# Performance work log

Hardware: AMD Instinct MI355X
Metric: run time of the kernel (lower is better)

The kernel has to match this reference:

```python
import jax, jax.numpy as jnp
import numpy as np

N, IN_DIM, H, K = 4096, 64, 64, 3
DT = 0.05


def graph_filter(z, S_powers, W):
    # z: [N, d_in], S_powers: [K, N, N], W: [K, d_in, d_out]
    zk = jnp.einsum('knm,md->knd', S_powers, z)   # K-hop diffused features
    return jnp.einsum('knd,kde->ne', zk, W)       # sum over taps k


def setup_inputs() -> dict:
    key = jax.random.key(0)
    ks = jax.random.split(key, 8)
    w_scale = 0.1
    return {
        'x': jax.random.normal(ks[0], (N, H), jnp.float32),
        'u': jax.random.normal(ks[1], (N, IN_DIM), jnp.float32),
        'S_powers': jax.random.normal(ks[2], (K, N, N), jnp.float32) / np.float32(np.sqrt(N)),
        'WA_hat': jax.random.normal(ks[3], (K, H, H), jnp.float32) * w_scale,
        'WB_hat': jax.random.normal(ks[4], (K, IN_DIM, H), jnp.float32) * w_scale,
        'WA_state': jax.random.normal(ks[5], (K, H, H), jnp.float32) * w_scale,
        'WB_state': jax.random.normal(ks[6], (K, IN_DIM, H), jnp.float32) * w_scale,
        'bx': jnp.zeros((1, H), jnp.float32),
        'bu': jnp.zeros((1, H), jnp.float32),
        'b': jnp.ones((1, H), jnp.float32) * 0.1,
        'n_steps': 4,
    }


def reference(x, u, S_powers, WA_hat, WB_hat, WA_state, WB_state, bx, bu, b, n_steps):
    # Input-driven terms are constant across solver steps; hoist them.
    fu = jax.nn.relu(graph_filter(u, S_powers, WB_hat) + bu)   # [N, H]
    sigma_c = jnp.tanh(graph_filter(u, S_powers, WB_state))    # [N, H]

    def step(xc, _):
        f = jax.nn.relu(graph_filter(xc, S_powers, WA_hat) + bx) + fu
        dx = -(b + f) * xc - graph_filter(xc, S_powers, WA_state) + f * sigma_c
        xn = jnp.clip(xc + DT * dx, -1.0, 1.0)
        return xn, None

    xf, _ = jax.lax.scan(step, x, None, length=n_steps)
    return xf
```

## Files before the change

kernel.cpp:

```cpp
#include <hip/hip_runtime.h>
#include <math.h>


typedef unsigned short u16;
typedef unsigned int u32;
typedef __attribute__((ext_vector_type(8))) short short8;
typedef __attribute__((ext_vector_type(4))) float f32x4;

#define NN 4096
#define HD 64
#define KB32 128
#define DT_C 0.05f

__device__ __forceinline__ u16 f2bf(float f) {
    u32 u = __float_as_uint(f);
    u += 0x7FFFu + ((u >> 16) & 1u);
    return (u16)(u >> 16);
}
__device__ __forceinline__ u32 pk2(float a, float b) {
    return (u32)f2bf(a) | ((u32)f2bf(b) << 16);
}

__global__ __launch_bounds__(256) void convS_kernel(
    const float* __restrict__ S, u16* __restrict__ SbT)
{
    const int slab = blockIdx.y;
    const int tap = slab >> 7, kb = slab & 127;
    const int t = threadIdx.x;
    const int n = blockIdx.x * 64 + (t >> 2);
    const int kq = (t & 3) * 8;
    const float* src = S + ((size_t)tap * NN + n) * NN + kb * 32 + kq;
    float4 f0 = ((const float4*)src)[0];
    float4 f1 = ((const float4*)src)[1];
    uint4 o;
    o.x = pk2(f0.x, f0.y); o.y = pk2(f0.z, f0.w);
    o.z = pk2(f1.x, f1.y); o.w = pk2(f1.z, f1.w);
    *(uint4*)(SbT + ((size_t)slab * NN + n) * 32 + kq) = o;
}

__global__ __launch_bounds__(256) void zprep_kernel(
    const float* __restrict__ u, const float* __restrict__ x,
    const float* __restrict__ WAh, const float* __restrict__ WAs,
    const float* __restrict__ WBh, const float* __restrict__ WBs,
    u16* __restrict__ utT, u16* __restrict__ xtT, u16* __restrict__ WtT)
{
    const int b = blockIdx.x;
    const int t = threadIdx.x;
    if (b < 256) {
        const float* z = (b < 128) ? u : x;
        u16* ztT = (b < 128) ? utT : xtT;
        const int kb = b & 127, n0 = kb * 32;
        __shared__ __align__(16) u16 tile[64][40];
        const int nl = t >> 3, c0 = (t & 7) * 8;
        const float* src = z + (size_t)(n0 + nl) * HD + c0;
        float4 f0 = ((const float4*)src)[0];
        float4 f1 = ((const float4*)src)[1];
        tile[c0 + 0][nl] = f2bf(f0.x); tile[c0 + 1][nl] = f2bf(f0.y);
        tile[c0 + 2][nl] = f2bf(f0.z); tile[c0 + 3][nl] = f2bf(f0.w);
        tile[c0 + 4][nl] = f2bf(f1.x); tile[c0 + 5][nl] = f2bf(f1.y);
        tile[c0 + 6][nl] = f2bf(f1.z); tile[c0 + 7][nl] = f2bf(f1.w);
        __syncthreads();
        const int e = t >> 2, kw0 = (t & 3) * 8;
        short8 v = *(const short8*)&tile[e][kw0];
        *(short8*)(ztT + ((size_t)kb * 64 + e) * 32 + kw0) = v;
    } else {
        for (int f = t; f < 4 * 6 * 64 * 32; f += 256) {
            int mat = f / 12288, r = f % 12288;
            int s = r / 2048, r2 = r % 2048;
            int e = r2 >> 5, kw = r2 & 31;
            int kp = s * 32 + kw, tap = kp >> 6, d = kp & 63;
            const float* Wm = (mat == 0) ? WAh : (mat == 1) ? WAs : (mat == 2) ? WBh : WBs;
            WtT[f] = f2bf(Wm[((size_t)tap * HD + d) * HD + e]);
        }
    }
}

__global__ __launch_bounds__(256) void pack_kernel(
    const float* __restrict__ xn, u16* __restrict__ xtT)
{
    const int kb = blockIdx.x, n0 = kb * 32;
    const int t = threadIdx.x;
    __shared__ __align__(16) u16 tile[64][40];
    const int nl = t >> 3, c0 = (t & 7) * 8;
    const float* src = xn + (size_t)(n0 + nl) * HD + c0;
    float4 f0 = ((const float4*)src)[0];
    float4 f1 = ((const float4*)src)[1];
    tile[c0 + 0][nl] = f2bf(f0.x); tile[c0 + 1][nl] = f2bf(f0.y);
    tile[c0 + 2][nl] = f2bf(f0.z); tile[c0 + 3][nl] = f2bf(f0.w);
    tile[c0 + 4][nl] = f2bf(f1.x); tile[c0 + 5][nl] = f2bf(f1.y);
    tile[c0 + 6][nl] = f2bf(f1.z); tile[c0 + 7][nl] = f2bf(f1.w);
    __syncthreads();
    const int e = t >> 2, kw0 = (t & 3) * 8;
    short8 v = *(const short8*)&tile[e][kw0];
    *(short8*)(xtT + ((size_t)kb * 64 + e) * 32 + kw0) = v;
}

__global__ __launch_bounds__(256) void diffuseA_kernel(
    const u16* __restrict__ SbT, const u16* __restrict__ utT,
    const u16* __restrict__ xtT, float* __restrict__ Yp, int iters)
{
    const int t = threadIdx.x;
    const int tap = blockIdx.z;
    const int row0 = blockIdx.x * 128;
    const int kb0 = blockIdx.y * iters;
    const int w = t >> 6, lane = t & 63, l15 = lane & 15, quad = lane >> 4;

    const u16* A0 = SbT + (((size_t)(tap * KB32) * NN + row0 + w * 32 + l15) * 32) + quad * 8;
    const size_t arowstride = (size_t)NN * 32;
    const u16* Bu = utT + (size_t)(l15)*0;

    f32x4 z4 = {0.f, 0.f, 0.f, 0.f};
    f32x4 acc[2][2][4];
    #pragma unroll
    for (int s = 0; s < 2; ++s)
        #pragma unroll
        for (int i = 0; i < 2; ++i)
            #pragma unroll
            for (int j = 0; j < 4; ++j) acc[s][i][j] = z4;

    #pragma unroll 2
    for (int it = 0; it < iters; ++it) {
        const int kb = kb0 + it;
        const u16* ab = A0 + (size_t)kb * arowstride;
        short8 a0 = *(const short8*)(ab);
        short8 a1 = *(const short8*)(ab + 16 * 32);
        #pragma unroll
        for (int ct = 0; ct < 4; ++ct) {
            const size_t bo = ((size_t)kb * 64 + ct * 16 + l15) * 32 + quad * 8;
            short8 bu = *(const short8*)(utT + bo);
            short8 bx = *(const short8*)(xtT + bo);
            acc[0][0][ct] = __builtin_amdgcn_mfma_f32_16x16x32_bf16(a0, bu, acc[0][0][ct], 0, 0, 0);
            acc[0][1][ct] = __builtin_amdgcn_mfma_f32_16x16x32_bf16(a1, bu, acc[0][1][ct], 0, 0, 0);
            acc[1][0][ct] = __builtin_amdgcn_mfma_f32_16x16x32_bf16(a0, bx, acc[1][0][ct], 0, 0, 0);
            acc[1][1][ct] = __builtin_amdgcn_mfma_f32_16x16x32_bf16(a1, bx, acc[1][1][ct], 0, 0, 0);
        }
    }
    (void)Bu;
    #pragma unroll
    for (int s = 0; s < 2; ++s) {
        float* yb = Yp + ((size_t)((blockIdx.y * 3 + tap) * 2 + s) * NN + row0) * HD;
        #pragma unroll
        for (int rt = 0; rt < 2; ++rt)
            #pragma unroll
            for (int ct = 0; ct < 4; ++ct)
                #pragma unroll
                for (int r = 0; r < 4; ++r)
                    yb[(size_t)(w * 32 + rt * 16 + quad * 4 + r) * HD + ct * 16 + l15] = acc[s][rt][ct][r];
    }
}

__global__ __launch_bounds__(256) void diffuseS_kernel(
    const u16* __restrict__ SbT, const u16* __restrict__ xtT,
    float* __restrict__ Yp, int iters)
{
    const int t = threadIdx.x;
    const int tap = blockIdx.z;
    const int row0 = blockIdx.x * 128;
    const int kb0 = blockIdx.y * iters;
    const int w = t >> 6, lane = t & 63, l15 = lane & 15, quad = lane >> 4;

    const u16* A0 = SbT + (((size_t)(tap * KB32) * NN + row0 + w * 32 + l15) * 32) + quad * 8;
    const size_t arowstride = (size_t)NN * 32;

    f32x4 z4 = {0.f, 0.f, 0.f, 0.f};
    f32x4 acc[2][4];
    #pragma unroll
    for (int i = 0; i < 2; ++i)
        #pragma unroll
        for (int j = 0; j < 4; ++j) acc[i][j] = z4;

    #pragma unroll 2
    for (int it = 0; it < iters; ++it) {
        const int kb = kb0 + it;
        const u16* ab = A0 + (size_t)kb * arowstride;
        short8 a0 = *(const short8*)(ab);
        short8 a1 = *(const short8*)(ab + 16 * 32);
        #pragma unroll
        for (int ct = 0; ct < 4; ++ct) {
            short8 bb = *(const short8*)(xtT + ((size_t)kb * 64 + ct * 16 + l15) * 32 + quad * 8);
            acc[0][ct] = __builtin_amdgcn_mfma_f32_16x16x32_bf16(a0, bb, acc[0][ct], 0, 0, 0);
            acc[1][ct] = __builtin_amdgcn_mfma_f32_16x16x32_bf16(a1, bb, acc[1][ct], 0, 0, 0);
        }
    }
    float* yb = Yp + ((size_t)(blockIdx.y * 3 + tap) * NN + row0) * HD;
    #pragma unroll
    for (int rt = 0; rt < 2; ++rt)
        #pragma unroll
        for (int ct = 0; ct < 4; ++ct)
            #pragma unroll
            for (int r = 0; r < 4; ++r)
                yb[(size_t)(w * 32 + rt * 16 + quad * 4 + r) * HD + ct * 16 + l15] = acc[rt][ct][r];
}

__global__ __launch_bounds__(256) void reduce_kernel(
    const float* __restrict__ Yp, int KS, int nsrc,
    u16* __restrict__ dst0, u16* __restrict__ dst1)
{
    const int tg = blockIdx.x * 256 + threadIdx.x;
    const int src = tg / 98304;
    const int r = tg - src * 98304;
    const int tap = r >> 15;
    const int r2 = r & 32767;
    const int n = r2 >> 3;
    const int dg = (r2 & 7) * 8;
    const float* p = Yp + (((size_t)tap * nsrc + src) * NN + n) * HD + dg;
    const size_t kstride = (size_t)3 * nsrc * NN * HD;
    float4 s0 = {0.f, 0.f, 0.f, 0.f}, s1 = {0.f, 0.f, 0.f, 0.f};
    for (int ks = 0; ks < KS; ++ks) {
        float4 v0 = ((const float4*)(p + ks * kstride))[0];
        float4 v1 = ((const float4*)(p + ks * kstride))[1];
        s0.x += v0.x; s0.y += v0.y; s0.z += v0.z; s0.w += v0.w;
        s1.x += v1.x; s1.y += v1.y; s1.z += v1.z; s1.w += v1.w;
    }
    u16* dst = src ? dst1 : dst0;
    uint4 o;
    o.x = pk2(s0.x, s0.y); o.y = pk2(s0.z, s0.w);
    o.z = pk2(s1.x, s1.y); o.w = pk2(s1.z, s1.w);
    *(uint4*)(dst + (((size_t)(tap * 2 + (dg >> 5)) * NN + n) * 32) + (dg & 31)) = o;
}

__global__ __launch_bounds__(64) void update_step_kernel(
    const u16* __restrict__ YxT, const u16* __restrict__ WtT,
    const float* __restrict__ bx, const float* __restrict__ bvec,
    const float* __restrict__ fu, const float* __restrict__ sc,
    const float* __restrict__ xc, float* __restrict__ xn)
{
    const int n0 = blockIdx.x * 16;
    const int lane = threadIdx.x, l15 = lane & 15, quad = lane >> 4;

    f32x4 z4 = {0.f, 0.f, 0.f, 0.f};
    f32x4 aF[4], aG[4];
    #pragma unroll
    for (int ct = 0; ct < 4; ++ct) { aF[ct] = z4; aG[ct] = z4; }
    #pragma unroll
    for (int s = 0; s < 6; ++s) {
        short8 a = *(const short8*)(YxT + (((size_t)s * NN + n0 + l15) * 32) + quad * 8);
        #pragma unroll
        for (int ct = 0; ct < 4; ++ct) {
            const size_t wo = (((size_t)(0 * 6 + s) * 64) + ct * 16 + l15) * 32 + quad * 8;
            short8 bF = *(const short8*)(WtT + wo);
            short8 bG = *(const short8*)(WtT + wo + 6 * 64 * 32);
            aF[ct] = __builtin_amdgcn_mfma_f32_16x16x32_bf16(a, bF, aF[ct], 0, 0, 0);
            aG[ct] = __builtin_amdgcn_mfma_f32_16x16x32_bf16(a, bG, aG[ct], 0, 0, 0);
        }
    }
    #pragma unroll
    for (int ct = 0; ct < 4; ++ct) {
        const int e = ct * 16 + l15;
        const float bxv = bx[e], bbv = bvec[e];
        #pragma unroll
        for (int r = 0; r < 4; ++r) {
            const int n = n0 + quad * 4 + r;
            const size_t o = (size_t)n * HD + e;
            float f = fmaxf(aF[ct][r] + bxv, 0.f) + fu[o];
            float g = aG[ct][r];
            float xv = xc[o];
            float dx = -(bbv + f) * xv - g + f * sc[o];
            xn[o] = fminf(fmaxf(xv + DT_C * dx, -1.f), 1.f);
        }
    }
}

__global__ __launch_bounds__(64) void update1_kernel(
    const u16* __restrict__ YuT, const u16* __restrict__ YxT,
    const u16* __restrict__ WtT,
    const float* __restrict__ bx, const float* __restrict__ bu,
    const float* __restrict__ bvec, const float* __restrict__ x0,
    float* __restrict__ fu, float* __restrict__ sc, float* __restrict__ x1)
{
    const int n0 = blockIdx.x * 16;
    const int lane = threadIdx.x, l15 = lane & 15, quad = lane >> 4;

    f32x4 z4 = {0.f, 0.f, 0.f, 0.f};
    f32x4 aFu[4], aSc[4], aF[4], aG[4];
    #pragma unroll
    for (int ct = 0; ct < 4; ++ct) { aFu[ct] = z4; aSc[ct] = z4; aF[ct] = z4; aG[ct] = z4; }
    #pragma unroll
    for (int s = 0; s < 6; ++s) {
        const size_t ao = (((size_t)s * NN + n0 + l15) * 32) + quad * 8;
        short8 au = *(const short8*)(YuT + ao);
        short8 ax = *(const short8*)(YxT + ao);
        #pragma unroll
        for (int ct = 0; ct < 4; ++ct) {
            const size_t wo = (((size_t)s * 64) + ct * 16 + l15) * 32 + quad * 8;
            short8 bF  = *(const short8*)(WtT + wo);
            short8 bG  = *(const short8*)(WtT + wo + 6 * 64 * 32);
            short8 bFu = *(const short8*)(WtT + wo + 2 * 6 * 64 * 32);
            short8 bSc = *(const short8*)(WtT + wo + 3 * 6 * 64 * 32);
            aF[ct]  = __builtin_amdgcn_mfma_f32_16x16x32_bf16(ax, bF,  aF[ct],  0, 0, 0);
            aG[ct]  = __builtin_amdgcn_mfma_f32_16x16x32_bf16(ax, bG,  aG[ct],  0, 0, 0);
            aFu[ct] = __builtin_amdgcn_mfma_f32_16x16x32_bf16(au, bFu, aFu[ct], 0, 0, 0);
            aSc[ct] = __builtin_amdgcn_mfma_f32_16x16x32_bf16(au, bSc, aSc[ct], 0, 0, 0);
        }
    }
    #pragma unroll
    for (int ct = 0; ct < 4; ++ct) {
        const int e = ct * 16 + l15;
        const float bxv = bx[e], buv = bu[e], bbv = bvec[e];
        #pragma unroll
        for (int r = 0; r < 4; ++r) {
            const int n = n0 + quad * 4 + r;
            const size_t o = (size_t)n * HD + e;
            float fuv = fmaxf(aFu[ct][r] + buv, 0.f);
            float scv = tanhf(aSc[ct][r]);
            float f = fmaxf(aF[ct][r] + bxv, 0.f) + fuv;
            float g = aG[ct][r];
            float xv = x0[o];
            float dx = -(bbv + f) * xv - g + f * scv;
            fu[o] = fuv; sc[o] = scv;
            x1[o] = fminf(fmaxf(xv + DT_C * dx, -1.f), 1.f);
        }
    }
}

extern "C" void kernel_launch(void* const* d_in, const int* in_sizes, int n_in,
                              void* d_out, int out_size, void* d_ws, size_t ws_size,
                              hipStream_t stream) {
    const float* x   = (const float*)d_in[0];
    const float* u   = (const float*)d_in[1];
    const float* S   = (const float*)d_in[2];
    const float* WAh = (const float*)d_in[3];
    const float* WBh = (const float*)d_in[4];
    const float* WAs = (const float*)d_in[5];
    const float* WBs = (const float*)d_in[6];
    const float* bx  = (const float*)d_in[7];
    const float* bu  = (const float*)d_in[8];
    const float* bvec= (const float*)d_in[9];
    float* out = (float*)d_out;

    const size_t sbf_bytes = (size_t)3 * NN * NN * 2;
    const size_t slice = (size_t)NN * HD * 4;
    const size_t rest = 2 * 524288 + 98304 + 2 * 1572864 + 4 * 1048576;
    int KS_A = 4, KS_S = 8;
    if (ws_size < sbf_bytes + 24 * slice + rest) { KS_A = 2; KS_S = 4; }
    if (ws_size < sbf_bytes + 12 * slice + rest) { KS_A = 1; KS_S = 2; }
    const int nslice = (KS_A * 6 > KS_S * 3) ? KS_A * 6 : KS_S * 3;

    char* p = (char*)d_ws;
    u16* SbT  = (u16*)p;         p += sbf_bytes;
    float* Yp = (float*)p;       p += (size_t)nslice * slice;
    u16* utT  = (u16*)p;         p += 524288;
    u16* xtT  = (u16*)p;         p += 524288;
    u16* WtT  = (u16*)p;         p += 98304;
    u16* YuT  = (u16*)p;         p += 1572864;
    u16* YxT  = (u16*)p;         p += 1572864;
    float* fu = (float*)p;       p += 1048576;
    float* sc = (float*)p;       p += 1048576;
    float* xA = (float*)p;       p += 1048576;
    float* xB = (float*)p;       p += 1048576;

    zprep_kernel<<<257, 256, 0, stream>>>(u, x, WAh, WAs, WBh, WBs, utT, xtT, WtT);
    convS_kernel<<<dim3(64, 384), 256, 0, stream>>>(S, SbT);

    diffuseA_kernel<<<dim3(32, KS_A, 3), 256, 0, stream>>>(SbT, utT, xtT, Yp, KB32 / KS_A);
    reduce_kernel<<<768, 256, 0, stream>>>(Yp, KS_A, 2, YuT, YxT);
    update1_kernel<<<256, 64, 0, stream>>>(YuT, YxT, WtT, bx, bu, bvec, x, fu, sc, xA);
    pack_kernel<<<128, 256, 0, stream>>>(xA, xtT);
    diffuseS_kernel<<<dim3(32, KS_S, 3), 256, 0, stream>>>(SbT, xtT, Yp, KB32 / KS_S);
    reduce_kernel<<<384, 256, 0, stream>>>(Yp, KS_S, 1, YxT, YxT);
    update_step_kernel<<<256, 64, 0, stream>>>(YxT, WtT, bx, bvec, fu, sc, xA, xB);
    pack_kernel<<<128, 256, 0, stream>>>(xB, xtT);

    diffuseS_kernel<<<dim3(32, KS_S, 3), 256, 0, stream>>>(SbT, xtT, Yp, KB32 / KS_S);
    reduce_kernel<<<384, 256, 0, stream>>>(Yp, KS_S, 1, YxT, YxT);
    update_step_kernel<<<256, 64, 0, stream>>>(YxT, WtT, bx, bvec, fu, sc, xB, xA);
    pack_kernel<<<128, 256, 0, stream>>>(xA, xtT);

    diffuseS_kernel<<<dim3(32, KS_S, 3), 256, 0, stream>>>(SbT, xtT, Yp, KB32 / KS_S);
    reduce_kernel<<<384, 256, 0, stream>>>(Yp, KS_S, 1, YxT, YxT);
    update_step_kernel<<<256, 64, 0, stream>>>(YxT, WtT, bx, bvec, fu, sc, xA, out);
}
```

Before: 534.8 us.

## Fuse S conversion into first diffusion and reduce/pack into update kernels

The separate fp32→bf16 conversion of S is folded into the first diffusion kernel, which reads fp32 S directly, converts it in registers, feeds MFMA and writes the bf16 copy for later steps. The split-K reduce and the bf16 repack of the new state are folded into the update kernels, which now use 256 threads, stage partial sums in LDS and write the packed transposed x themselves. This removes several launches and intermediate round-trips through global memory. In exchange the first diffusion kernel becomes heavier on memory traffic and conversion work, and each update block redoes the split-K sum for its own rows.

Result: faster. 491.6 us (-8.1%).

```diff
diff --git a/kernel.cpp b/kernel.cpp
--- a/kernel.cpp
+++ b/kernel.cpp
@@ -19,23 +19,6 @@
 }
 __device__ __forceinline__ u32 pk2(float a, float b) {
     return (u32)f2bf(a) | ((u32)f2bf(b) << 16);
-}
-
-__global__ __launch_bounds__(256) void convS_kernel(
-    const float* __restrict__ S, u16* __restrict__ SbT)
-{
-    const int slab = blockIdx.y;
-    const int tap = slab >> 7, kb = slab & 127;
-    const int t = threadIdx.x;
-    const int n = blockIdx.x * 64 + (t >> 2);
-    const int kq = (t & 3) * 8;
-    const float* src = S + ((size_t)tap * NN + n) * NN + kb * 32 + kq;
-    float4 f0 = ((const float4*)src)[0];
-    float4 f1 = ((const float4*)src)[1];
-    uint4 o;
-    o.x = pk2(f0.x, f0.y); o.y = pk2(f0.z, f0.w);
-    o.z = pk2(f1.x, f1.y); o.w = pk2(f1.z, f1.w);
-    *(uint4*)(SbT + ((size_t)slab * NN + n) * 32 + kq) = o;
 }
 
 __global__ __launch_bounds__(256) void zprep_kernel(
@@ -75,29 +58,10 @@
     }
 }
 
-__global__ __launch_bounds__(256) void pack_kernel(
-    const float* __restrict__ xn, u16* __restrict__ xtT)
-{
-    const int kb = blockIdx.x, n0 = kb * 32;
-    const int t = threadIdx.x;
-    __shared__ __align__(16) u16 tile[64][40];
-    const int nl = t >> 3, c0 = (t & 7) * 8;
-    const float* src = xn + (size_t)(n0 + nl) * HD + c0;
-    float4 f0 = ((const float4*)src)[0];
-    float4 f1 = ((const float4*)src)[1];
-    tile[c0 + 0][nl] = f2bf(f0.x); tile[c0 + 1][nl] = f2bf(f0.y);
-    tile[c0 + 2][nl] = f2bf(f0.z); tile[c0 + 3][nl] = f2bf(f0.w);
-    tile[c0 + 4][nl] = f2bf(f1.x); tile[c0 + 5][nl] = f2bf(f1.y);
-    tile[c0 + 6][nl] = f2bf(f1.z); tile[c0 + 7][nl] = f2bf(f1.w);
-    __syncthreads();
-    const int e = t >> 2, kw0 = (t & 3) * 8;
-    short8 v = *(const short8*)&tile[e][kw0];
-    *(short8*)(xtT + ((size_t)kb * 64 + e) * 32 + kw0) = v;
-}
-
 __global__ __launch_bounds__(256) void diffuseA_kernel(
-    const u16* __restrict__ SbT, const u16* __restrict__ utT,
-    const u16* __restrict__ xtT, float* __restrict__ Yp, int iters)
+    const float* __restrict__ S, const u16* __restrict__ utT,
+    const u16* __restrict__ xtT, u16* __restrict__ SbT,
+    float* __restrict__ Yp, int iters)
 {
     const int t = threadIdx.x;
     const int tap = blockIdx.z;
@@ -105,9 +69,9 @@
     const int kb0 = blockIdx.y * iters;
     const int w = t >> 6, lane = t & 63, l15 = lane & 15, quad = lane >> 4;
 
-    const u16* A0 = SbT + (((size_t)(tap * KB32) * NN + row0 + w * 32 + l15) * 32) + quad * 8;
-    const size_t arowstride = (size_t)NN * 32;
-    const u16* Bu = utT + (size_t)(l15)*0;
+    const int r0 = row0 + w * 32 + l15;
+    const float* Sb = S + ((size_t)tap * NN + r0) * NN + quad * 8;
+    u16* Wb = SbT + (((size_t)tap * KB32) * NN + r0) * 32 + quad * 8;
 
     f32x4 z4 = {0.f, 0.f, 0.f, 0.f};
     f32x4 acc[2][2][4];
@@ -117,6 +81,68 @@
         for (int i = 0; i < 2; ++i)
             #pragma unroll
             for (int j = 0; j < 4; ++j) acc[s][i][j] = z4;
+
+    #pragma unroll 2
+    for (int it = 0; it < iters; ++it) {
+        const int kb = kb0 + it;
+        const float* sp0 = Sb + (size_t)kb * 32;
+        const float* sp1 = sp0 + (size_t)16 * NN;
+        float4 f0 = ((const float4*)sp0)[0];
+        float4 f1 = ((const float4*)sp0)[1];
+        float4 g0 = ((const float4*)sp1)[0];
+        float4 g1 = ((const float4*)sp1)[1];
+        union U { uint4 u4; short8 s8; };
+        U A0, A1;
+        A0.u4.x = pk2(f0.x, f0.y); A0.u4.y = pk2(f0.z, f0.w);
+        A0.u4.z = pk2(f1.x, f1.y); A0.u4.w = pk2(f1.z, f1.w);
+        A1.u4.x = pk2(g0.x, g0.y); A1.u4.y = pk2(g0.z, g0.w);
+        A1.u4.z = pk2(g1.x, g1.y); A1.u4.w = pk2(g1.z, g1.w);
+        u16* wb = Wb + (size_t)kb * (NN * 32);
+        *(uint4*)wb = A0.u4;
+        *(uint4*)(wb + 16 * 32) = A1.u4;
+        #pragma unroll
+        for (int ct = 0; ct < 4; ++ct) {
+            const size_t bo = ((size_t)kb * 64 + ct * 16 + l15) * 32 + quad * 8;
+            short8 bu = *(const short8*)(utT + bo);
+            short8 bx = *(const short8*)(xtT + bo);
+            acc[0][0][ct] = __builtin_amdgcn_mfma_f32_16x16x32_bf16(A0.s8, bu, acc[0][0][ct], 0, 0, 0);
+            acc[0][1][ct] = __builtin_amdgcn_mfma_f32_16x16x32_bf16(A1.s8, bu, acc[0][1][ct], 0, 0, 0);
+            acc[1][0][ct] = __builtin_amdgcn_mfma_f32_16x16x32_bf16(A0.s8, bx, acc[1][0][ct], 0, 0, 0);
+            acc[1][1][ct] = __builtin_amdgcn_mfma_f32_16x16x32_bf16(A1.s8, bx, acc[1][1][ct], 0, 0, 0);
+        }
+    }
+    #pragma unroll
+    for (int s = 0; s < 2; ++s) {
+        float* yb = Yp + ((size_t)((blockIdx.y * 3 + tap) * 2 + s) * NN + row0) * HD;
+        #pragma unroll
+        for (int rt = 0; rt < 2; ++rt)
+            #pragma unroll
+            for (int ct = 0; ct < 4; ++ct)
+                #pragma unroll
+                for (int r = 0; r < 4; ++r)
+                    yb[(size_t)(w * 32 + rt * 16 + quad * 4 + r) * HD + ct * 16 + l15] = acc[s][rt][ct][r];
+    }
+}
+
+__global__ __launch_bounds__(256) void diffuseS_kernel(
+    const u16* __restrict__ SbT, const u16* __restrict__ xtT,
+    float* __restrict__ Yp, int iters)
+{
+    const int t = threadIdx.x;
+    const int tap = blockIdx.z;
+    const int row0 = blockIdx.x * 128;
+    const int kb0 = blockIdx.y * iters;
+    const int w = t >> 6, lane = t & 63, l15 = lane & 15, quad = lane >> 4;
+
+    const u16* A0 = SbT + (((size_t)(tap * KB32) * NN + row0 + w * 32 + l15) * 32) + quad * 8;
+    const size_t arowstride = (size_t)NN * 32;
+
+    f32x4 z4 = {0.f, 0.f, 0.f, 0.f};
+    f32x4 acc[2][4];
+    #pragma unroll
+    for (int i = 0; i < 2; ++i)
+        #pragma unroll
+        for (int j = 0; j < 4; ++j) acc[i][j] = z4;
 
     #pragma unroll 2
     for (int it = 0; it < iters; ++it) {
@@ -126,57 +152,6 @@
         short8 a1 = *(const short8*)(ab + 16 * 32);
         #pragma unroll
         for (int ct = 0; ct < 4; ++ct) {
-            const size_t bo = ((size_t)kb * 64 + ct * 16 + l15) * 32 + quad * 8;
-            short8 bu = *(const short8*)(utT + bo);
-            short8 bx = *(const short8*)(xtT + bo);
-            acc[0][0][ct] = __builtin_amdgcn_mfma_f32_16x16x32_bf16(a0, bu, acc[0][0][ct], 0, 0, 0);
-            acc[0][1][ct] = __builtin_amdgcn_mfma_f32_16x16x32_bf16(a1, bu, acc[0][1][ct], 0, 0, 0);
-            acc[1][0][ct] = __builtin_amdgcn_mfma_f32_16x16x32_bf16(a0, bx, acc[1][0][ct], 0, 0, 0);
-            acc[1][1][ct] = __builtin_amdgcn_mfma_f32_16x16x32_bf16(a1, bx, acc[1][1][ct], 0, 0, 0);
-        }
-    }
-    (void)Bu;
-    #pragma unroll
-    for (int s = 0; s < 2; ++s) {
-        float* yb = Yp + ((size_t)((blockIdx.y * 3 + tap) * 2 + s) * NN + row0) * HD;
-        #pragma unroll
-        for (int rt = 0; rt < 2; ++rt)
-            #pragma unroll
-            for (int ct = 0; ct < 4; ++ct)
-                #pragma unroll
-                for (int r = 0; r < 4; ++r)
-                    yb[(size_t)(w * 32 + rt * 16 + quad * 4 + r) * HD + ct * 16 + l15] = acc[s][rt][ct][r];
-    }
-}
-
-__global__ __launch_bounds__(256) void diffuseS_kernel(
-    const u16* __restrict__ SbT, const u16* __restrict__ xtT,
-    float* __restrict__ Yp, int iters)
-{
-    const int t = threadIdx.x;
-    const int tap = blockIdx.z;
-    const int row0 = blockIdx.x * 128;
-    const int kb0 = blockIdx.y * iters;
-    const int w = t >> 6, lane = t & 63, l15 = lane & 15, quad = lane >> 4;
-
-    const u16* A0 = SbT + (((size_t)(tap * KB32) * NN + row0 + w * 32 + l15) * 32) + quad * 8;
-    const size_t arowstride = (size_t)NN * 32;
-
-    f32x4 z4 = {0.f, 0.f, 0.f, 0.f};
-    f32x4 acc[2][4];
-    #pragma unroll
-    for (int i = 0; i < 2; ++i)
-        #pragma unroll
-        for (int j = 0; j < 4; ++j) acc[i][j] = z4;
-
-    #pragma unroll 2
-    for (int it = 0; it < iters; ++it) {
-        const int kb = kb0 + it;
-        const u16* ab = A0 + (size_t)kb * arowstride;
-        short8 a0 = *(const short8*)(ab);
-        short8 a1 = *(const short8*)(ab + 16 * 32);
-        #pragma unroll
-        for (int ct = 0; ct < 4; ++ct) {
             short8 bb = *(const short8*)(xtT + ((size_t)kb * 64 + ct * 16 + l15) * 32 + quad * 8);
             acc[0][ct] = __builtin_amdgcn_mfma_f32_16x16x32_bf16(a0, bb, acc[0][ct], 0, 0, 0);
             acc[1][ct] = __builtin_amdgcn_mfma_f32_16x16x32_bf16(a1, bb, acc[1][ct], 0, 0, 0);
@@ -192,123 +167,163 @@
                 yb[(size_t)(w * 32 + rt * 16 + quad * 4 + r) * HD + ct * 16 + l15] = acc[rt][ct][r];
 }
 
-__global__ __launch_bounds__(256) void reduce_kernel(
-    const float* __restrict__ Yp, int KS, int nsrc,
-    u16* __restrict__ dst0, u16* __restrict__ dst1)
-{
-    const int tg = blockIdx.x * 256 + threadIdx.x;
-    const int src = tg / 98304;
-    const int r = tg - src * 98304;
-    const int tap = r >> 15;
-    const int r2 = r & 32767;
-    const int n = r2 >> 3;
-    const int dg = (r2 & 7) * 8;
-    const float* p = Yp + (((size_t)tap * nsrc + src) * NN + n) * HD + dg;
-    const size_t kstride = (size_t)3 * nsrc * NN * HD;
-    float4 s0 = {0.f, 0.f, 0.f, 0.f}, s1 = {0.f, 0.f, 0.f, 0.f};
-    for (int ks = 0; ks < KS; ++ks) {
-        float4 v0 = ((const float4*)(p + ks * kstride))[0];
-        float4 v1 = ((const float4*)(p + ks * kstride))[1];
-        s0.x += v0.x; s0.y += v0.y; s0.z += v0.z; s0.w += v0.w;
-        s1.x += v1.x; s1.y += v1.y; s1.z += v1.z; s1.w += v1.w;
-    }
-    u16* dst = src ? dst1 : dst0;
-    uint4 o;
-    o.x = pk2(s0.x, s0.y); o.y = pk2(s0.z, s0.w);
-    o.z = pk2(s1.x, s1.y); o.w = pk2(s1.z, s1.w);
-    *(uint4*)(dst + (((size_t)(tap * 2 + (dg >> 5)) * NN + n) * 32) + (dg & 31)) = o;
-}
-
-__global__ __launch_bounds__(64) void update_step_kernel(
-    const u16* __restrict__ YxT, const u16* __restrict__ WtT,
+__global__ __launch_bounds__(256) void update_step_kernel(
+    const float* __restrict__ Yp, int KS, const u16* __restrict__ WtT,
     const float* __restrict__ bx, const float* __restrict__ bvec,
     const float* __restrict__ fu, const float* __restrict__ sc,
-    const float* __restrict__ xc, float* __restrict__ xn)
-{
+    const float* __restrict__ xc, float* __restrict__ xn,
+    u16* __restrict__ xtT, int do_pack)
+{
+    __shared__ __align__(16) u16 yt[6][16][56];
+    __shared__ __align__(16) u16 pkt[64][24];
+    const int t = threadIdx.x;
     const int n0 = blockIdx.x * 16;
-    const int lane = threadIdx.x, l15 = lane & 15, quad = lane >> 4;
-
+
+    for (int f = t; f < 384; f += 256) {
+        const int tap = f >> 7;
+        const int r = f & 127;
+        const int nl = r >> 3, d8 = r & 7, d0 = d8 * 8;
+        const float* p = Yp + ((size_t)tap * NN + n0 + nl) * HD + d0;
+        const size_t kstride = (size_t)3 * NN * HD;
+        float4 s0 = {0.f, 0.f, 0.f, 0.f}, s1 = {0.f, 0.f, 0.f, 0.f};
+        for (int y = 0; y < KS; ++y) {
+            float4 v0 = ((const float4*)(p + (size_t)y * kstride))[0];
+            float4 v1 = ((const float4*)(p + (size_t)y * kstride))[1];
+            s0.x += v0.x; s0.y += v0.y; s0.z += v0.z; s0.w += v0.w;
+            s1.x += v1.x; s1.y += v1.y; s1.z += v1.z; s1.w += v1.w;
+        }
+        uint4 o;
+        o.x = pk2(s0.x, s0.y); o.y = pk2(s0.z, s0.w);
+        o.z = pk2(s1.x, s1.y); o.w = pk2(s1.z, s1.w);
+        const int s = tap * 2 + (d8 >> 2), kw0 = (d8 & 3) * 8;
+        *(uint4*)&yt[s][nl][kw0] = o;
+    }
+    __syncthreads();
+
+    const int wv = t >> 6, lane = t & 63, l15 = lane & 15, quad = lane >> 4;
     f32x4 z4 = {0.f, 0.f, 0.f, 0.f};
-    f32x4 aF[4], aG[4];
-    #pragma unroll
-    for (int ct = 0; ct < 4; ++ct) { aF[ct] = z4; aG[ct] = z4; }
+    f32x4 aF = z4, aG = z4;
     #pragma unroll
     for (int s = 0; s < 6; ++s) {
-        short8 a = *(const short8*)(YxT + (((size_t)s * NN + n0 + l15) * 32) + quad * 8);
-        #pragma unroll
-        for (int ct = 0; ct < 4; ++ct) {
-            const size_t wo = (((size_t)(0 * 6 + s) * 64) + ct * 16 + l15) * 32 + quad * 8;
-            short8 bF = *(const short8*)(WtT + wo);
-            short8 bG = *(const short8*)(WtT + wo + 6 * 64 * 32);
-            aF[ct] = __builtin_amdgcn_mfma_f32_16x16x32_bf16(a, bF, aF[ct], 0, 0, 0);
-            aG[ct] = __builtin_amdgcn_mfma_f32_16x16x32_bf16(a, bG, aG[ct], 0, 0, 0);
-        }
-    }
-    #pragma unroll
-    for (int ct = 0; ct < 4; ++ct) {
-        const int e = ct * 16 + l15;
-        const float bxv = bx[e], bbv = bvec[e];
-        #pragma unroll
-        for (int r = 0; r < 4; ++r) {
-            const int n = n0 + quad * 4 + r;
-            const size_t o = (size_t)n * HD + e;
-            float f = fmaxf(aF[ct][r] + bxv, 0.f) + fu[o];
-            float g = aG[ct][r];
-            float xv = xc[o];
-            float dx = -(bbv + f) * xv - g + f * sc[o];
-            xn[o] = fminf(fmaxf(xv + DT_C * dx, -1.f), 1.f);
-        }
-    }
-}
-
-__global__ __launch_bounds__(64) void update1_kernel(
-    const u16* __restrict__ YuT, const u16* __restrict__ YxT,
-    const u16* __restrict__ WtT,
+        short8 a = *(const short8*)&yt[s][l15][quad * 8];
+        const size_t wo = ((size_t)s * 64 + wv * 16 + l15) * 32 + quad * 8;
+        short8 bF = *(const short8*)(WtT + wo);
+        short8 bG = *(const short8*)(WtT + wo + 12288);
+        aF = __builtin_amdgcn_mfma_f32_16x16x32_bf16(a, bF, aF, 0, 0, 0);
+        aG = __builtin_amdgcn_mfma_f32_16x16x32_bf16(a, bG, aG, 0, 0, 0);
+    }
+    const int e = wv * 16 + l15;
+    const float bxv = bx[e], bbv = bvec[e];
+    float xos[4];
+    #pragma unroll
+    for (int r = 0; r < 4; ++r) {
+        const int n = n0 + quad * 4 + r;
+        const size_t o = (size_t)n * HD + e;
+        float ff = fmaxf(aF[r] + bxv, 0.f) + fu[o];
+        float xv = xc[o];
+        float dx = -(bbv + ff) * xv - aG[r] + ff * sc[o];
+        float xo = fminf(fmaxf(xv + DT_C * dx, -1.f), 1.f);
+        xn[o] = xo;
+        xos[r] = xo;
+    }
+    if (do_pack) {
+        uint2 pv;
+        pv.x = pk2(xos[0], xos[1]);
+        pv.y = pk2(xos[2], xos[3]);
+        *(uint2*)&pkt[e][quad * 4] = pv;
+        __syncthreads();
+        if (t < 128) {
+            const int ee = t >> 1, g = t & 1;
+            short8 v = *(const short8*)&pkt[ee][g * 8];
+            const int kb = n0 >> 5;
+            const int kwb = (n0 & 31) + g * 8;
+            *(short8*)(xtT + ((size_t)kb * 64 + ee) * 32 + kwb) = v;
+        }
+    }
+}
+
+__global__ __launch_bounds__(256) void update1_kernel(
+    const float* __restrict__ Yp, int KS, const u16* __restrict__ WtT,
     const float* __restrict__ bx, const float* __restrict__ bu,
     const float* __restrict__ bvec, const float* __restrict__ x0,
-    float* __restrict__ fu, float* __restrict__ sc, float* __restrict__ x1)
-{
+    float* __restrict__ fu, float* __restrict__ sc, float* __restrict__ x1,
+    u16* __restrict__ xtT)
+{
+    __shared__ __align__(16) u16 yt[2][6][16][56];
+    __shared__ __align__(16) u16 pkt[64][24];
+    const int t = threadIdx.x;
     const int n0 = blockIdx.x * 16;
-    const int lane = threadIdx.x, l15 = lane & 15, quad = lane >> 4;
-
+
+    #pragma unroll
+    for (int ff = 0; ff < 3; ++ff) {
+        const int f = t + ff * 256;
+        const int src = f / 384;
+        const int r3 = f - src * 384;
+        const int tap = r3 >> 7;
+        const int r = r3 & 127;
+        const int nl = r >> 3, d8 = r & 7, d0 = d8 * 8;
+        const float* p = Yp + (((size_t)(tap * 2 + src)) * NN + n0 + nl) * HD + d0;
+        const size_t kstride = (size_t)6 * NN * HD;
+        float4 s0 = {0.f, 0.f, 0.f, 0.f}, s1 = {0.f, 0.f, 0.f, 0.f};
+        for (int y = 0; y < KS; ++y) {
+            float4 v0 = ((const float4*)(p + (size_t)y * kstride))[0];
+            float4 v1 = ((const float4*)(p + (size_t)y * kstride))[1];
+            s0.x += v0.x; s0.y += v0.y; s0.z += v0.z; s0.w += v0.w;
+            s1.x += v1.x; s1.y += v1.y; s1.z += v1.z; s1.w += v1.w;
+        }
+        uint4 o;
+        o.x = pk2(s0.x, s0.y); o.y = pk2(s0.z, s0.w);
+        o.z = pk2(s1.x, s1.y); o.w = pk2(s1.z, s1.w);
+        const int s = tap * 2 + (d8 >> 2), kw0 = (d8 & 3) * 8;
+        *(uint4*)&yt[src][s][nl][kw0] = o;
+    }
+    __syncthreads();
+
+    const int wv = t >> 6, lane = t & 63, l15 = lane & 15, quad = lane >> 4;
     f32x4 z4 = {0.f, 0.f, 0.f, 0.f};
-    f32x4 aFu[4], aSc[4], aF[4], aG[4];
-    #pragma unroll
-    for (int ct = 0; ct < 4; ++ct) { aFu[ct] = z4; aSc[ct] = z4; aF[ct] = z4; aG[ct] = z4; }
+    f32x4 aF = z4, aG = z4, aFu = z4, aSc = z4;
     #pragma unroll
     for (int s = 0; s < 6; ++s) {
-        const size_t ao = (((size_t)s * NN + n0 + l15) * 32) + quad * 8;
-        short8 au = *(const short8*)(YuT + ao);
-        short8 ax = *(const short8*)(YxT + ao);
-        #pragma unroll
-        for (int ct = 0; ct < 4; ++ct) {
-            const size_t wo = (((size_t)s * 64) + ct * 16 + l15) * 32 + quad * 8;
-            short8 bF  = *(const short8*)(WtT + wo);
-            short8 bG  = *(const short8*)(WtT + wo + 6 * 64 * 32);
-            short8 bFu = *(const short8*)(WtT + wo + 2 * 6 * 64 * 32);
-            short8 bSc = *(const short8*)(WtT + wo + 3 * 6 * 64 * 32);
-            aF[ct]  = __builtin_amdgcn_mfma_f32_16x16x32_bf16(ax, bF,  aF[ct],  0, 0, 0);
-            aG[ct]  = __builtin_amdgcn_mfma_f32_16x16x32_bf16(ax, bG,  aG[ct],  0, 0, 0);
-            aFu[ct] = __builtin_amdgcn_mfma_f32_16x16x32_bf16(au, bFu, aFu[ct], 0, 0, 0);
-            aSc[ct] = __builtin_amdgcn_mfma_f32_16x16x32_bf16(au, bSc, aSc[ct], 0, 0, 0);
-        }
-    }
-    #pragma unroll
-    for (int ct = 0; ct < 4; ++ct) {
-        const int e = ct * 16 + l15;
-        const float bxv = bx[e], buv = bu[e], bbv = bvec[e];
-        #pragma unroll
-        for (int r = 0; r < 4; ++r) {
-            const int n = n0 + quad * 4 + r;
-            const size_t o = (size_t)n * HD + e;
-            float fuv = fmaxf(aFu[ct][r] + buv, 0.f);
-            float scv = tanhf(aSc[ct][r]);
-            float f = fmaxf(aF[ct][r] + bxv, 0.f) + fuv;
-            float g = aG[ct][r];
-            float xv = x0[o];
-            float dx = -(bbv + f) * xv - g + f * scv;
-            fu[o] = fuv; sc[o] = scv;
-            x1[o] = fminf(fmaxf(xv + DT_C * dx, -1.f), 1.f);
+        short8 au = *(const short8*)&yt[0][s][l15][quad * 8];
+        short8 ax = *(const short8*)&yt[1][s][l15][quad * 8];
+        const size_t wo = ((size_t)s * 64 + wv * 16 + l15) * 32 + quad * 8;
+        short8 bF  = *(const short8*)(WtT + wo);
+        short8 bG  = *(const short8*)(WtT + wo + 12288);
+        short8 bFu = *(const short8*)(WtT + wo + 2 * 12288);
+        short8 bSc = *(const short8*)(WtT + wo + 3 * 12288);
+        aF  = __builtin_amdgcn_mfma_f32_16x16x32_bf16(ax, bF,  aF,  0, 0, 0);
+        aG  = __builtin_amdgcn_mfma_f32_16x16x32_bf16(ax, bG,  aG,  0, 0, 0);
+        aFu = __builtin_amdgcn_mfma_f32_16x16x32_bf16(au, bFu, aFu, 0, 0, 0);
+        aSc = __builtin_amdgcn_mfma_f32_16x16x32_bf16(au, bSc, aSc, 0, 0, 0);
+    }
+    const int e = wv * 16 + l15;
+    const float bxv = bx[e], buv = bu[e], bbv = bvec[e];
+    float xos[4];
+    #pragma unroll
+    for (int r = 0; r < 4; ++r) {
+        const int n = n0 + quad * 4 + r;
+        const size_t o = (size_t)n * HD + e;
+        float fuv = fmaxf(aFu[r] + buv, 0.f);
+        float scv = tanhf(aSc[r]);
+        float ff = fmaxf(aF[r] + bxv, 0.f) + fuv;
+        float xv = x0[o];
+        float dx = -(bbv + ff) * xv - aG[r] + ff * scv;
+        float xo = fminf(fmaxf(xv + DT_C * dx, -1.f), 1.f);
+        fu[o] = fuv; sc[o] = scv; x1[o] = xo;
+        xos[r] = xo;
+    }
+    {
+        uint2 pv;
+        pv.x = pk2(xos[0], xos[1]);
+        pv.y = pk2(xos[2], xos[3]);
+        *(uint2*)&pkt[e][quad * 4] = pv;
+        __syncthreads();
+        if (t < 128) {
+            const int ee = t >> 1, g = t & 1;
+            short8 v = *(const short8*)&pkt[ee][g * 8];
+            const int kb = n0 >> 5;
+            const int kwb = (n0 & 31) + g * 8;
+            *(short8*)(xtT + ((size_t)kb * 64 + ee) * 32 + kwb) = v;
         }
     }
 }
@@ -330,11 +345,10 @@
 
     const size_t sbf_bytes = (size_t)3 * NN * NN * 2;
     const size_t slice = (size_t)NN * HD * 4;
-    const size_t rest = 2 * 524288 + 98304 + 2 * 1572864 + 4 * 1048576;
-    int KS_A = 4, KS_S = 8;
-    if (ws_size < sbf_bytes + 24 * slice + rest) { KS_A = 2; KS_S = 4; }
-    if (ws_size < sbf_bytes + 12 * slice + rest) { KS_A = 1; KS_S = 2; }
-    const int nslice = (KS_A * 6 > KS_S * 3) ? KS_A * 6 : KS_S * 3;
+    const size_t rest = 2 * 524288 + 98304 + 4 * 1048576;
+    int KS_A = 4, KS_S = 8, nslice = 24;
+    if (ws_size < sbf_bytes + 24 * slice + rest) { KS_A = 2; KS_S = 4; nslice = 12; }
+    if (ws_size < sbf_bytes + 12 * slice + rest) { KS_A = 1; KS_S = 2; nslice = 6; }
 
     char* p = (char*)d_ws;
     u16* SbT  = (u16*)p;         p += sbf_bytes;
@@ -342,31 +356,22 @@
     u16* utT  = (u16*)p;         p += 524288;
     u16* xtT  = (u16*)p;         p += 524288;
     u16* WtT  = (u16*)p;         p += 98304;
-    u16* YuT  = (u16*)p;         p += 1572864;
-    u16* YxT  = (u16*)p;         p += 1572864;
     float* fu = (float*)p;       p += 1048576;
     float* sc = (float*)p;       p += 1048576;
     float* xA = (float*)p;       p += 1048576;
     float* xB = (float*)p;       p += 1048576;
 
     zprep_kernel<<<257, 256, 0, stream>>>(u, x, WAh, WAs, WBh, WBs, utT, xtT, WtT);
-    convS_kernel<<<dim3(64, 384), 256, 0, stream>>>(S, SbT);
-
-    diffuseA_kernel<<<dim3(32, KS_A, 3), 256, 0, stream>>>(SbT, utT, xtT, Yp, KB32 / KS_A);
-    reduce_kernel<<<768, 256, 0, stream>>>(Yp, KS_A, 2, YuT, YxT);
-    update1_kernel<<<256, 64, 0, stream>>>(YuT, YxT, WtT, bx, bu, bvec, x, fu, sc, xA);
-    pack_kernel<<<128, 256, 0, stream>>>(xA, xtT);
+
+    diffuseA_kernel<<<dim3(32, KS_A, 3), 256, 0, stream>>>(S, utT, xtT, SbT, Yp, KB32 / KS_A);
+    update1_kernel<<<256, 256, 0, stream>>>(Yp, KS_A, WtT, bx, bu, bvec, x, fu, sc, xA, xtT);
+
     diffuseS_kernel<<<dim3(32, KS_S, 3), 256, 0, stream>>>(SbT, xtT, Yp, KB32 / KS_S);
-    reduce_kernel<<<384, 256, 0, stream>>>(Yp, KS_S, 1, YxT, YxT);
-    update_step_kernel<<<256, 64, 0, stream>>>(YxT, WtT, bx, bvec, fu, sc, xA, xB);
-    pack_kernel<<<128, 256, 0, stream>>>(xB, xtT);
+    update_step_kernel<<<256, 256, 0, stream>>>(Yp, KS_S, WtT, bx, bvec, fu, sc, xA, xB, xtT, 1);
 
     diffuseS_kernel<<<dim3(32, KS_S, 3), 256, 0, stream>>>(SbT, xtT, Yp, KB32 / KS_S);
-    reduce_kernel<<<384, 256, 0, stream>>>(Yp, KS_S, 1, YxT, YxT);
-    update_step_kernel<<<256, 64, 0, stream>>>(YxT, WtT, bx, bvec, fu, sc, xB, xA);
-    pack_kernel<<<128, 256, 0, stream>>>(xA, xtT);
+    update_step_kernel<<<256, 256, 0, stream>>>(Yp, KS_S, WtT, bx, bvec, fu, sc, xB, xA, xtT, 1);
 
     diffuseS_kernel<<<dim3(32, KS_S, 3), 256, 0, stream>>>(SbT, xtT, Yp, KB32 / KS_S);
-    reduce_kernel<<<384, 256, 0, stream>>>(Yp, KS_S, 1, YxT, YxT);
-    update_step_kernel<<<256, 64, 0, stream>>>(YxT, WtT, bx, bvec, fu, sc, xA, out);
-}
+    update_step_kernel<<<256, 256, 0, stream>>>(Yp, KS_S, WtT, bx, bvec, fu, sc, xA, out, xtT, 0);
+}
```
